# Kernel optimization log

Measured on AMD Instinct MI355X. Metric: run time of the kernel, lower is better.

Reference implementation:

```python
import jax, jax.numpy as jnp
import numpy as np

H = 16  # num heads


def setup_inputs() -> dict:
    key = jax.random.key(0)
    k1, k2, k3 = jax.random.split(key, 3)
    L, N, E = 2048, 4, 1024
    x = jax.random.normal(k1, (L, N, E), dtype=jnp.float32)
    wqkv = jax.random.normal(k2, (3 * E, E), dtype=jnp.float32) * 0.02
    wout = jax.random.normal(k3, (E, E), dtype=jnp.float32) * 0.02
    return {"x": x, "wqkv": wqkv, "wout": wout}


def reference(x, wqkv, wout):
    L, N, E = x.shape
    d = E // H
    scale = d ** (-0.5)
    # qkv projection: [L, N, 3E]
    qkv = jnp.einsum('lne,fe->lnf', x, wqkv)
    q, k, v = jnp.split(qkv, 3, axis=-1)
    # reshape to [N*H, L, d]
    def to_bld(t):
        return t.reshape(L, N * H, d).transpose(1, 0, 2)
    q = to_bld(q) * scale
    k = to_bld(k)
    v = to_bld(v)
    # full LxL scores (faithful to the naive implementation)
    attn = jnp.einsum('bld,bmd->blm', q, k)  # [N*H, L, L]
    causal = jnp.tril(jnp.ones((L, L), dtype=bool))
    attn = jnp.where(causal[None, :, :], attn, jnp.float32(-10000.0))
    attn = jax.nn.softmax(attn, axis=-1)
    # dropout = 0.0 / eval mode -> no-op
    out = jnp.einsum('blm,bmd->bld', attn, v)  # [N*H, L, d]
    out = out.transpose(1, 0, 2).reshape(L, N, E)
    out = jnp.einsum('lne,fe->lnf', out, wout)
    return jnp.sum(out)
```

## Files before the change

### kernel.cpp

```cpp
#include <hip/hip_runtime.h>
#include <hip/hip_bf16.h>

#define LSEQ 2048
#define NB   4
#define EMB  1024
#define NH   16
#define DH   64
#define BH   (NB*NH)
#define SCALE 0.125f
#define CCH  8
#define LOG2E 1.4426950408889634f
#define NEG16LOG2E (-23.083120654223414f)

typedef unsigned short ushort8 __attribute__((ext_vector_type(8)));
typedef __attribute__((ext_vector_type(8))) short bf16x8;
typedef __attribute__((ext_vector_type(4))) float f32x4;
typedef __attribute__((ext_vector_type(16))) float f32x16;
typedef __attribute__((ext_vector_type(2))) float f32x2;

#define EXP2F(x) __builtin_amdgcn_exp2f(x)

#define WAITV4  asm volatile("s_waitcnt vmcnt(4)" ::: "memory")
#define WAITV0  asm volatile("s_waitcnt vmcnt(0)" ::: "memory")
#define RBAR    asm volatile("s_barrier" ::: "memory")

__device__ __forceinline__ unsigned short f_to_bf(float f) {
    unsigned int u = __float_as_uint(f);
    return (unsigned short)((u + 0x7fffu + ((u >> 16) & 1u)) >> 16);
}

__device__ __forceinline__ void gload_lds16(const void* g, void* l) {
    __builtin_amdgcn_global_load_lds(
        (const __attribute__((address_space(1))) unsigned int*)g,
        (__attribute__((address_space(3))) unsigned int*)l, 16, 0, 0);
}

__global__ __launch_bounds__(256) void prep_kernel(const float* __restrict__ wqkv,
                                                   const float* __restrict__ wout,
                                                   unsigned short* __restrict__ wb,
                                                   float* __restrict__ wpart) {
    if (blockIdx.x < 1024) {
        int i = blockIdx.x * 256 + threadIdx.x;
        const float4* p = reinterpret_cast<const float4*>(wqkv) + (size_t)i * 2;
        float4 a = p[0], b = p[1];
        ushort8 o;
        o[0] = f_to_bf(a.x); o[1] = f_to_bf(a.y); o[2] = f_to_bf(a.z); o[3] = f_to_bf(a.w);
        o[4] = f_to_bf(b.x); o[5] = f_to_bf(b.y); o[6] = f_to_bf(b.z); o[7] = f_to_bf(b.w);
        reinterpret_cast<ushort8*>(wb)[i] = o;
    } else {
        int bb = blockIdx.x - 1024;
        int fc = bb >> 2;
        int e  = (bb & 3) * 256 + threadIdx.x;
        float s = 0.f;
        #pragma unroll 8
        for (int f = fc * 32; f < fc * 32 + 32; ++f) s += wout[(size_t)f * EMB + e];
        wpart[(size_t)fc * EMB + e] = s;
    }
}

__global__ __launch_bounds__(256) void wveff_kernel(const float* __restrict__ wqkv,
                                                    const float* __restrict__ wpart,
                                                    float* __restrict__ wveff) {
    __shared__ float psum[4][64];
    __shared__ float ws[64];
    const int tid = threadIdx.x;
    const int h   = blockIdx.x >> 2;
    {
        int v = tid & 63, q = tid >> 6;
        float s = 0.f;
        #pragma unroll
        for (int cc = q * 8; cc < q * 8 + 8; ++cc)
            s += wpart[(size_t)cc * EMB + h * 64 + v];
        psum[q][v] = s;
    }
    __syncthreads();
    if (tid < 64) ws[tid] = psum[0][tid] + psum[1][tid] + psum[2][tid] + psum[3][tid];
    __syncthreads();
    int e = (blockIdx.x & 3) * 256 + tid;
    float s = 0.f;
    #pragma unroll 8
    for (int j = 0; j < 64; ++j)
        s += wqkv[(size_t)(2 * EMB + h * 64 + j) * EMB + e] * ws[j];
    wveff[h * EMB + e] = s;
}

__global__ __launch_bounds__(256) void vw_kernel(const float* __restrict__ x,
                                                 const float* __restrict__ wveff,
                                                 float* __restrict__ vw,
                                                 unsigned short* __restrict__ xb) {
    int wave = threadIdx.x >> 6;
    int lane = threadIdx.x & 63;
    int r0 = blockIdx.x * 16 + wave;
    float acc0[NH] = {}, acc1[NH] = {}, acc2[NH] = {}, acc3[NH] = {};
    for (int e = lane; e < EMB; e += 64) {
        float xe0 = x[(size_t)r0 * EMB + e];
        float xe1 = x[(size_t)(r0 + 4) * EMB + e];
        float xe2 = x[(size_t)(r0 + 8) * EMB + e];
        float xe3 = x[(size_t)(r0 + 12) * EMB + e];
        xb[(size_t)r0 * EMB + e]        = f_to_bf(xe0);
        xb[(size_t)(r0 + 4) * EMB + e]  = f_to_bf(xe1);
        xb[(size_t)(r0 + 8) * EMB + e]  = f_to_bf(xe2);
        xb[(size_t)(r0 + 12) * EMB + e] = f_to_bf(xe3);
        #pragma unroll
        for (int h = 0; h < NH; ++h) {
            float wv = wveff[h * EMB + e];
            acc0[h] += xe0 * wv;
            acc1[h] += xe1 * wv;
            acc2[h] += xe2 * wv;
            acc3[h] += xe3 * wv;
        }
    }
    #pragma unroll
    for (int h = 0; h < NH; ++h) {
        float v0 = acc0[h], v1 = acc1[h], v2 = acc2[h], v3 = acc3[h];
        #pragma unroll
        for (int off = 32; off > 0; off >>= 1) {
            v0 += __shfl_down(v0, off, 64);
            v1 += __shfl_down(v1, off, 64);
            v2 += __shfl_down(v2, off, 64);
            v3 += __shfl_down(v3, off, 64);
        }
        if (lane == 0) {
            #pragma unroll
            for (int rr = 0; rr < 4; ++rr) {
                int r = r0 + rr * 4;
                float v = (rr == 0) ? v0 : (rr == 1) ? v1 : (rr == 2) ? v2 : v3;
                vw[(size_t)((r & 3) * NH + h) * LSEQ + (r >> 2)] = v;
            }
        }
    }
}

#define PBM 128
#define PBN 128
#define PBK 64
#define BUFS ((PBM + PBN) * PBK)

__device__ __forceinline__ void proj_stage(const unsigned short* __restrict__ xb,
                                           const unsigned short* __restrict__ wb,
                                           unsigned short* As, unsigned short* Bs,
                                           int r0, int c0, int k0, int wid, int srow, int sj) {
    #pragma unroll
    for (int i = 0; i < 2; ++i) {
        int seg = wid * 2 + i;
        gload_lds16(&xb[(size_t)(r0 + seg * 8 + srow) * EMB + k0 + sj], &As[seg * 8 * PBK]);
        gload_lds16(&wb[(size_t)(c0 + seg * 8 + srow) * EMB + k0 + sj], &Bs[seg * 8 * PBK]);
    }
}

__device__ __forceinline__ void proj_compute(const unsigned short* As, const unsigned short* Bs,
                                             int wr, int wc, int col, int g, f32x4 (&acc)[4][2]) {
    #pragma unroll
    for (int kk = 0; kk < 2; ++kk) {
        bf16x8 af[4], bff[2];
        #pragma unroll
        for (int m = 0; m < 4; ++m) {
            int row = wr * 64 + m * 16 + col;
            af[m] = *reinterpret_cast<const bf16x8*>(
                &As[row * PBK + (((kk * 4 + g) ^ (row & 7)) * 8)]);
        }
        #pragma unroll
        for (int n = 0; n < 2; ++n) {
            int row = wc * 32 + n * 16 + col;
            bff[n] = *reinterpret_cast<const bf16x8*>(
                &Bs[row * PBK + (((kk * 4 + g) ^ (row & 7)) * 8)]);
        }
        #pragma unroll
        for (int m = 0; m < 4; ++m)
            #pragma unroll
            for (int n = 0; n < 2; ++n)
                acc[m][n] = __builtin_amdgcn_mfma_f32_16x16x32_bf16(af[m], bff[n], acc[m][n], 0, 0, 0);
    }
}

__global__ __launch_bounds__(512) void proj_mfma(const unsigned short* __restrict__ xb,
                                                 const unsigned short* __restrict__ wb,
                                                 unsigned short* __restrict__ qws,
                                                 unsigned short* __restrict__ kws) {
    __shared__ unsigned short SMEM[2 * BUFS];
    unsigned short* As0 = SMEM;
    unsigned short* Bs0 = SMEM + PBM * PBK;
    unsigned short* As1 = SMEM + BUFS;
    unsigned short* Bs1 = As1 + PBM * PBK;
    const int tid  = threadIdx.x;
    const int lane = tid & 63;
    const int wid  = tid >> 6;
    const int wr   = wid >> 2, wc = wid & 3;
    const int d  = blockIdx.x;
    const int w  = (d & 7) * 128 + (d >> 3);
    const int r0 = (w >> 4) * PBM;
    const int c0 = (w & 15) * PBN;
    const int col  = lane & 15, g = lane >> 4;

    f32x4 acc[4][2];
    #pragma unroll
    for (int m = 0; m < 4; ++m)
        #pragma unroll
        for (int n = 0; n < 2; ++n) acc[m][n] = f32x4{0.f, 0.f, 0.f, 0.f};

    const int srow = lane >> 3;
    const int sj   = ((lane & 7) ^ (lane >> 3)) * 8;

    proj_stage(xb, wb, As0, Bs0, r0, c0, 0, wid, srow, sj);
    WAITV0; RBAR;
    #pragma unroll 1
    for (int t = 0; t < 16; t += 2) {
        proj_stage(xb, wb, As1, Bs1, r0, c0, (t + 1) * PBK, wid, srow, sj);
        WAITV4; RBAR;
        proj_compute(As0, Bs0, wr, wc, col, g, acc);
        RBAR;
        if (t + 2 < 16) {
            proj_stage(xb, wb, As0, Bs0, r0, c0, (t + 2) * PBK, wid, srow, sj);
            WAITV4;
        } else {
            WAITV0;
        }
        RBAR;
        proj_compute(As1, Bs1, wr, wc, col, g, acc);
        RBAR;
    }

    const float scl = (c0 < EMB) ? SCALE * LOG2E : 1.0f;
    #pragma unroll
    for (int m = 0; m < 4; ++m) {
        #pragma unroll
        for (int n = 0; n < 2; ++n) {
            #pragma unroll
            for (int j = 0; j < 4; ++j) {
                int row = wr * 64 + m * 16 + g * 4 + j;
                int cc  = wc * 32 + n * 16 + col;
                SMEM[row * 128 + (((cc >> 3) ^ (row & 7)) * 8) + (cc & 7)] =
                    f_to_bf(acc[m][n][j] * scl);
            }
        }
    }
    __syncthreads();
    #pragma unroll
    for (int pass = 0; pass < 4; ++pass) {
        int unit = pass * 64 + (tid >> 3);
        int r    = unit >> 1;
        int hsel = unit & 1;
        int pg   = (tid & 7) ^ (r & 7);
        ushort8 u = *reinterpret_cast<const ushort8*>(
            &SMEM[r * 128 + (hsel * 8 + (tid & 7)) * 8]);
        int rg = r0 + r;
        int nb = rg & 3, l = rg >> 2;
        int cbase = c0 + hsel * 64;
        unsigned short* dstp;
        if (c0 < EMB) {
            dstp = &qws[((size_t)(nb * NH + (cbase >> 6)) * LSEQ + l) * DH];
        } else {
            int c2 = cbase - EMB;
            dstp = &kws[((size_t)(nb * NH + (c2 >> 6)) * LSEQ + l) * DH];
        }
        *reinterpret_cast<ushort8*>(dstp + pg * 8) = u;
    }
}

__device__ __forceinline__ void lds_kfrag(const unsigned short* Ks, int ti, int m, int half,
                                          bf16x8* kf) {
    const char* base = reinterpret_cast<const char*>(Ks);
    #pragma unroll
    for (int kk = 0; kk < 4; ++kk) {
        int byte = ti * 4096 + m * 128 + ((half * 16 + kk * 32) ^ ((m & 7) << 4));
        kf[kk] = *reinterpret_cast<const bf16x8*>(base + byte);
    }
}
__device__ __forceinline__ f32x16 mfma_tile(const bf16x8* kf, const bf16x8* qf) {
    f32x16 acc;
    #pragma unroll
    for (int j = 0; j < 16; ++j) acc[j] = NEG16LOG2E;
    #pragma unroll
    for (int kk = 0; kk < 4; ++kk)
        acc = __builtin_amdgcn_mfma_f32_32x32x16_bf16(kf[kk], qf[kk], acc, 0, 0, 0);
    return acc;
}
__device__ __forceinline__ void expacc(const f32x16& acc, const float* vt, int half,
                                       f32x2& z2, f32x2& o2) {
    #pragma unroll
    for (int q = 0; q < 4; ++q) {
        float4 v4 = *reinterpret_cast<const float4*>(&vt[8 * q + 4 * half]);
        f32x2 p01 = {EXP2F(acc[4 * q + 0]), EXP2F(acc[4 * q + 1])};
        f32x2 p23 = {EXP2F(acc[4 * q + 2]), EXP2F(acc[4 * q + 3])};
        f32x2 v01 = {v4.x, v4.y};
        f32x2 v23 = {v4.z, v4.w};
        z2 += p01;
        o2 += p01 * v01;
        z2 += p23;
        o2 += p23 * v23;
    }
}
__device__ __forceinline__ void expacc_diag(const f32x16& acc, const float* vt, int half,
                                            int row, f32x2& z2, f32x2& o2) {
    #pragma unroll
    for (int q = 0; q < 4; ++q) {
        float4 v4 = *reinterpret_cast<const float4*>(&vt[8 * q + 4 * half]);
        float vvq[4] = {v4.x, v4.y, v4.z, v4.w};
        #pragma unroll
        for (int j = 0; j < 4; ++j) {
            int mrow = j + 8 * q + 4 * half;
            float p = EXP2F(acc[4 * q + j]);
            p = (mrow <= row) ? p : 0.f;
            z2[0] += p;
            o2[0] += p * vvq[j];
        }
    }
}

__global__ __launch_bounds__(512) void attn_mfma(const unsigned short* __restrict__ qws,
                                                 const unsigned short* __restrict__ kws,
                                                 const float* __restrict__ vw,
                                                 float2* __restrict__ zopart) {
    __shared__ unsigned short Ks[CCH * 2048];
    __shared__ float vt[CCH][32];
    const int tid = threadIdx.x;
    const int b   = blockIdx.x & 63;
    const int c   = blockIdx.x >> 6;

    {
        int ti = tid >> 6, lane = tid & 63;
        int row = lane >> 1, hb = lane & 1;
        const unsigned short* src = &kws[((size_t)b * LSEQ + (c + CCH * ti) * 32 + row) * DH + hb * 32];
        char* dst = reinterpret_cast<char*>(Ks) + ti * 4096 + row * 128;
        #pragma unroll
        for (int s = 0; s < 4; ++s) {
            ushort8 u = *reinterpret_cast<const ushort8*>(src + s * 8);
            *reinterpret_cast<ushort8*>(dst + ((hb * 64 + s * 16) ^ ((row & 7) << 4))) = u;
        }
        if (tid < 256) vt[tid >> 5][tid & 31] =
            vw[(size_t)b * LSEQ + (c + CCH * (tid >> 5)) * 32 + (tid & 31)];
    }
    __syncthreads();

    const int wid  = tid >> 6;
    const int lane = tid & 63;
    const int row  = lane & 31;
    const int half = lane >> 5;

    const unsigned short* qb_all = &qws[((size_t)b * LSEQ + row) * DH + 8 * half];
    bf16x8 qf[4], qn[4];
    #pragma unroll
    for (int kk = 0; kk < 4; ++kk)
        qf[kk] = *reinterpret_cast<const bf16x8*>(qb_all + (size_t)wid * 32 * DH + kk * 16);

    #pragma unroll
    for (int k = 0; k < 8; ++k) {
        const int lb = 8 * k + wid;
        if (k < 7) {
            const unsigned short* qnp = qb_all + (size_t)(lb + 8) * 32 * DH;
            #pragma unroll
            for (int kk = 0; kk < 4; ++kk)
                qn[kk] = *reinterpret_cast<const bf16x8*>(qnp + kk * 16);
        }
        const int nfull = (lb > c) ? ((lb - c + 7) >> 3) : 0;
        const bool has_diag = ((lb & 7) == c);
        f32x2 z2 = {0.f, 0.f}, o2 = {0.f, 0.f};
        if (nfull > 0 || has_diag) {
            int ti = 0;
            for (; ti + 1 < nfull; ti += 2) {
                bf16x8 ka[4], kc[4];
                lds_kfrag(Ks, ti, row, half, ka);
                lds_kfrag(Ks, ti + 1, row, half, kc);
                __builtin_amdgcn_s_setprio(1);
                f32x16 accA = mfma_tile(ka, qf);
                f32x16 accB = mfma_tile(kc, qf);
                __builtin_amdgcn_s_setprio(0);
                expacc(accA, &vt[ti][0], half, z2, o2);
                expacc(accB, &vt[ti + 1][0], half, z2, o2);
            }
            if (ti < nfull) {
                bf16x8 ka[4];
                lds_kfrag(Ks, ti, row, half, ka);
                f32x16 accA = mfma_tile(ka, qf);
                expacc(accA, &vt[ti][0], half, z2, o2);
            }
            if (has_diag) {
                const int td = nfull;
                bf16x8 ka[4];
                lds_kfrag(Ks, td, row, half, ka);
                f32x16 accA = mfma_tile(ka, qf);
                expacc_diag(accA, &vt[td][0], half, row, z2, o2);
            }
        }
        float z = z2[0] + z2[1];
        float o = o2[0] + o2[1];
        z += __shfl_xor(z, 32, 64);
        o += __shfl_xor(o, 32, 64);
        if (half == 0)
            zopart[((size_t)(b * 64 + lb) * CCH + c) * 32 + row] = float2{z, o};
        #pragma unroll
        for (int kk = 0; kk < 4; ++kk) qf[kk] = qn[kk];
    }
}

__global__ __launch_bounds__(256) void attn_combine(const float2* __restrict__ zopart,
                                                    float* __restrict__ partials) {
    __shared__ float red[256];
    const int t = threadIdx.x;
    const int e = blockIdx.x * 256 + t;
    const int bl = e >> 5, col = e & 31;
    float z = 0.f, o = 0.f;
    #pragma unroll
    for (int c = 0; c < CCH; ++c) {
        float2 p = zopart[((size_t)bl * CCH + c) * 32 + col];
        z += p.x; o += p.y;
    }
    red[t] = o / z;
    __syncthreads();
    for (int sh = 128; sh > 0; sh >>= 1) {
        if (t < sh) red[t] += red[t + sh];
        __syncthreads();
    }
    if (t == 0) partials[blockIdx.x] = red[0];
}

__global__ void reduce_kernel(const float* __restrict__ partials, float* __restrict__ out) {
    __shared__ float red[256];
    int t = threadIdx.x;
    red[t] = partials[t] + partials[t + 256];
    __syncthreads();
    for (int sh = 128; sh > 0; sh >>= 1) {
        if (t < sh) red[t] += red[t + sh];
        __syncthreads();
    }
    if (t == 0) out[0] = red[0];
}

extern "C" void kernel_launch(void* const* d_in, const int* in_sizes, int n_in,
                              void* d_out, int out_size, void* d_ws, size_t ws_size,
                              hipStream_t stream) {
    const float* x    = (const float*)d_in[0];
    const float* wqkv = (const float*)d_in[1];
    const float* wout = (const float*)d_in[2];
    float* out = (float*)d_out;

    unsigned short* qws = (unsigned short*)d_ws;
    unsigned short* kws = qws + (size_t)BH * LSEQ * DH;
    unsigned short* xb  = kws + (size_t)BH * LSEQ * DH;
    unsigned short* wb  = xb + (size_t)LSEQ * NB * EMB;
    float* vw       = (float*)(wb + (size_t)2 * EMB * EMB);
    float* wveff    = vw + (size_t)BH * LSEQ;
    float* partials = wveff + NH * EMB;
    float* wpart    = partials + 1024;
    float2* zopart  = (float2*)xb;

    hipLaunchKernelGGL(prep_kernel,   dim3(1024 + 128), dim3(256), 0, stream,
                       wqkv, wout, wb, wpart);
    hipLaunchKernelGGL(wveff_kernel,  dim3(NH * 4), dim3(256), 0, stream, wqkv, wpart, wveff);
    hipLaunchKernelGGL(vw_kernel,     dim3(LSEQ * NB / 16), dim3(256), 0, stream, x, wveff, vw, xb);
    hipLaunchKernelGGL(proj_mfma,     dim3(1024), dim3(512), 0, stream,
                       xb, wb, qws, kws);
    hipLaunchKernelGGL(attn_mfma,     dim3(BH * CCH), dim3(512), 0, stream,
                       qws, kws, vw, zopart);
    hipLaunchKernelGGL(attn_combine,  dim3(512), dim3(256), 0, stream, zopart, partials);
    hipLaunchKernelGGL(reduce_kernel, dim3(1), dim3(256), 0, stream, partials, out);
}
```

Before: 111.2 us.

## Process two query blocks per K fragment load to reuse LDS K and V reads

The attention loop now handles two query blocks (lb0, lb1) per pass and walks all eight K tiles, loading each K fragment and its V values from LDS once and applying them to both query blocks. V values are loaded into registers once per tile instead of inside every exp-accumulate call. This halves LDS reads of K per query block, but it drops the software prefetch of the next Q block, uses non-unrolled loops with per-tile causal branches, and raises register pressure from the two Q fragment sets and accumulators.

```diff
diff --git a/kernel.cpp b/kernel.cpp
--- a/kernel.cpp
+++ b/kernel.cpp
@@ -275,27 +275,25 @@
         acc = __builtin_amdgcn_mfma_f32_32x32x16_bf16(kf[kk], qf[kk], acc, 0, 0, 0);
     return acc;
 }
-__device__ __forceinline__ void expacc(const f32x16& acc, const float* vt, int half,
-                                       f32x2& z2, f32x2& o2) {
+__device__ __forceinline__ void expacc_r(const f32x16& acc, const float4* vv,
+                                         f32x2& z2, f32x2& o2) {
     #pragma unroll
     for (int q = 0; q < 4; ++q) {
-        float4 v4 = *reinterpret_cast<const float4*>(&vt[8 * q + 4 * half]);
         f32x2 p01 = {EXP2F(acc[4 * q + 0]), EXP2F(acc[4 * q + 1])};
         f32x2 p23 = {EXP2F(acc[4 * q + 2]), EXP2F(acc[4 * q + 3])};
-        f32x2 v01 = {v4.x, v4.y};
-        f32x2 v23 = {v4.z, v4.w};
+        f32x2 v01 = {vv[q].x, vv[q].y};
+        f32x2 v23 = {vv[q].z, vv[q].w};
         z2 += p01;
         o2 += p01 * v01;
         z2 += p23;
         o2 += p23 * v23;
     }
 }
-__device__ __forceinline__ void expacc_diag(const f32x16& acc, const float* vt, int half,
-                                            int row, f32x2& z2, f32x2& o2) {
+__device__ __forceinline__ void expacc_diag_r(const f32x16& acc, const float4* vv, int half,
+                                              int row, f32x2& z2, f32x2& o2) {
     #pragma unroll
     for (int q = 0; q < 4; ++q) {
-        float4 v4 = *reinterpret_cast<const float4*>(&vt[8 * q + 4 * half]);
-        float vvq[4] = {v4.x, v4.y, v4.z, v4.w};
+        float vvq[4] = {vv[q].x, vv[q].y, vv[q].z, vv[q].w};
         #pragma unroll
         for (int j = 0; j < 4; ++j) {
             int mrow = j + 8 * q + 4 * half;
@@ -338,58 +336,58 @@
     const int half = lane >> 5;
 
     const unsigned short* qb_all = &qws[((size_t)b * LSEQ + row) * DH + 8 * half];
-    bf16x8 qf[4], qn[4];
-    #pragma unroll
-    for (int kk = 0; kk < 4; ++kk)
-        qf[kk] = *reinterpret_cast<const bf16x8*>(qb_all + (size_t)wid * 32 * DH + kk * 16);
-
-    #pragma unroll
-    for (int k = 0; k < 8; ++k) {
-        const int lb = 8 * k + wid;
-        if (k < 7) {
-            const unsigned short* qnp = qb_all + (size_t)(lb + 8) * 32 * DH;
+
+    #pragma unroll 1
+    for (int p = 0; p < 4; ++p) {
+        const int k0 = 2 * p, k1 = 2 * p + 1;
+        const int lb0 = 8 * k0 + wid, lb1 = 8 * k1 + wid;
+        bf16x8 qfa[4], qfb[4];
+        {
+            const unsigned short* qa = qb_all + (size_t)lb0 * 32 * DH;
+            const unsigned short* qb = qb_all + (size_t)lb1 * 32 * DH;
             #pragma unroll
-            for (int kk = 0; kk < 4; ++kk)
-                qn[kk] = *reinterpret_cast<const bf16x8*>(qnp + kk * 16);
-        }
-        const int nfull = (lb > c) ? ((lb - c + 7) >> 3) : 0;
-        const bool has_diag = ((lb & 7) == c);
-        f32x2 z2 = {0.f, 0.f}, o2 = {0.f, 0.f};
-        if (nfull > 0 || has_diag) {
-            int ti = 0;
-            for (; ti + 1 < nfull; ti += 2) {
-                bf16x8 ka[4], kc[4];
-                lds_kfrag(Ks, ti, row, half, ka);
-                lds_kfrag(Ks, ti + 1, row, half, kc);
+            for (int kk = 0; kk < 4; ++kk) {
+                qfa[kk] = *reinterpret_cast<const bf16x8*>(qa + kk * 16);
+                qfb[kk] = *reinterpret_cast<const bf16x8*>(qb + kk * 16);
+            }
+        }
+        f32x2 z2a = {0.f, 0.f}, o2a = {0.f, 0.f};
+        f32x2 z2b = {0.f, 0.f}, o2b = {0.f, 0.f};
+
+        #pragma unroll 1
+        for (int ti = 0; ti < 8; ++ti) {
+            const int t = c + CCH * ti;
+            bf16x8 kf[4];
+            lds_kfrag(Ks, ti, row, half, kf);
+            float4 vv[4];
+            #pragma unroll
+            for (int q = 0; q < 4; ++q)
+                vv[q] = *reinterpret_cast<const float4*>(&vt[ti][8 * q + 4 * half]);
+            if (lb0 >= t) {
                 __builtin_amdgcn_s_setprio(1);
-                f32x16 accA = mfma_tile(ka, qf);
-                f32x16 accB = mfma_tile(kc, qf);
+                f32x16 accA = mfma_tile(kf, qfa);
                 __builtin_amdgcn_s_setprio(0);
-                expacc(accA, &vt[ti][0], half, z2, o2);
-                expacc(accB, &vt[ti + 1][0], half, z2, o2);
+                if (lb0 > t) expacc_r(accA, vv, z2a, o2a);
+                else         expacc_diag_r(accA, vv, half, row, z2a, o2a);
             }
-            if (ti < nfull) {
-                bf16x8 ka[4];
-                lds_kfrag(Ks, ti, row, half, ka);
-                f32x16 accA = mfma_tile(ka, qf);
-                expacc(accA, &vt[ti][0], half, z2, o2);
+            if (lb1 >= t) {
+                __builtin_amdgcn_s_setprio(1);
+                f32x16 accB = mfma_tile(kf, qfb);
+                __builtin_amdgcn_s_setprio(0);
+                if (lb1 > t) expacc_r(accB, vv, z2b, o2b);
+                else         expacc_diag_r(accB, vv, half, row, z2b, o2b);
             }
-            if (has_diag) {
-                const int td = nfull;
-                bf16x8 ka[4];
-                lds_kfrag(Ks, td, row, half, ka);
-                f32x16 accA = mfma_tile(ka, qf);
-                expacc_diag(accA, &vt[td][0], half, row, z2, o2);
-            }
-        }
-        float z = z2[0] + z2[1];
-        float o = o2[0] + o2[1];
-        z += __shfl_xor(z, 32, 64);
-        o += __shfl_xor(o, 32, 64);
-        if (half == 0)
-            zopart[((size_t)(b * 64 + lb) * CCH + c) * 32 + row] = float2{z, o};
-        #pragma unroll
-        for (int kk = 0; kk < 4; ++kk) qf[kk] = qn[kk];
+        }
+        float za = z2a[0] + z2a[1], oa = o2a[0] + o2a[1];
+        float zb = z2b[0] + z2b[1], ob = o2b[0] + o2b[1];
+        za += __shfl_xor(za, 32, 64);
+        oa += __shfl_xor(oa, 32, 64);
+        zb += __shfl_xor(zb, 32, 64);
+        ob += __shfl_xor(ob, 32, 64);
+        if (half == 0) {
+            zopart[((size_t)(b * 64 + lb0) * CCH + c) * 32 + row] = float2{za, oa};
+            zopart[((size_t)(b * 64 + lb1) * CCH + c) * 32 + row] = float2{zb, ob};
+        }
     }
 }
 
```

After: 112.5 us. About the same (+1.2%).
